# Performance work log

Hardware: AMD Instinct MI355X
Metric: run time of the kernel (lower is better)

The kernel has to match this reference:

```python
import jax, jax.numpy as jnp
import numpy as np

T = 32.0                       # softmax temperature
THRESH = float(np.cos(np.pi * 40.0 / 180.0))  # cos(degree), degree=40
NEG_INF = -9.0e15


def setup_inputs() -> dict:
    key = jax.random.key(0)
    ks = jax.random.split(key, 11)
    B, C, D_IMG, D_ATT, H_ATT, H = 2048, 1000, 2048, 312, 128, 128
    def rn(k, shape, scale=1.0):
        return jax.random.normal(k, shape, dtype=jnp.float32) * scale
    return {
        "image_feats": rn(ks[0], (B, D_IMG)),
        "img_proto":   rn(ks[1], (C, D_IMG)),
        "attributes":  rn(ks[2], (C, D_ATT)),
        "unused":      0,
        # parameters
        "att_g":   rn(ks[3], (D_ATT, H_ATT), 0.05),
        "slim_w":  rn(ks[4], (D_IMG, D_ATT), 0.02),   # proto_slim weight (transposed torch layout)
        "slim_b":  rn(ks[5], (D_ATT,), 0.02),
        "img_w":   rn(ks[6], (D_IMG, H), 0.02),
        "proto_w": rn(ks[7], (2 * D_ATT, H), 0.02),   # att_dim + proto_red_dim = 624
        "proto_b": rn(ks[8], (1, H), 0.02),
        "fc_w":    rn(ks[9], (H, 1), 0.05),
        "fc_b":    rn(ks[10], (1,), 0.05),
    }


def reference(image_feats, img_proto, attributes, unused,
              att_g, slim_w, slim_b, img_w, proto_w, proto_b, fc_w, fc_b):
    # proto_slim: [C, D_img] -> [C, att_dim]
    proto_red = img_proto @ slim_w + slim_b

    # --- get_attention: cosine similarity among attribute projections ---
    g = attributes @ att_g                                   # [C, att_hC] (g == h in original)
    gn = g / jnp.clip(jnp.linalg.norm(g, axis=1, keepdims=True), 1e-12)
    sim = gn @ gn.T                                          # [C, C] cosine similarity
    raw = jnp.where(sim > THRESH, sim, NEG_INF)              # threshold mask
    attn = jax.nn.softmax(raw * T, axis=1)                   # [C, C]

    # --- propagate prototypes ---
    att_outs = attn @ attributes                             # [C, att_dim]
    img_proto_outs = attn @ proto_red                        # [C, att_dim]
    outs = jnp.concatenate([att_outs, img_proto_outs], axis=1)  # [C, 2*att_dim]

    # --- relation MLP (broadcast instead of materialized expand+matmul) ---
    img_h = image_feats @ img_w                              # [B, H]
    proto_h = outs @ proto_w                                 # [C, H]
    hidden = jax.nn.relu(img_h[:, None, :] + proto_h[None, :, :] + proto_b)  # [B, C, H]
    outputs = hidden @ fc_w + fc_b                           # [B, C, 1]
    return outputs[..., 0]                                   # [B, C]
```

## Files before the change

kernel.cpp:

```cpp
#include <hip/hip_runtime.h>

typedef unsigned short ushort_t;
typedef __bf16 bf16x8 __attribute__((ext_vector_type(8)));
typedef float f32x4 __attribute__((ext_vector_type(4)));
typedef float f32x2 __attribute__((ext_vector_type(2)));
typedef ushort_t us4 __attribute__((ext_vector_type(4)));

#define T_SOFT 32.0f
#define THRESH 0.76604444311897803f
#define SW 1048
#define SO 648

__device__ __forceinline__ ushort_t f2bf(float f) {
  union { float f; unsigned u; } x; x.f = f;
  unsigned r = (x.u + 0x7fffu + ((x.u >> 16) & 1u)) >> 16;
  return (ushort_t)r;
}
__device__ __forceinline__ float bf2f(ushort_t h) {
  union { unsigned u; float f; } x; x.u = ((unsigned)h) << 16; return x.f;
}

__device__ __forceinline__ us4 pack4(float4 x) {
  union { unsigned u[2]; us4 h; } r;
  union { float4 f; unsigned u[4]; } a;
  a.f = x;
  r.u[0] = __builtin_amdgcn_perm(a.u[1] + 0x8000u, a.u[0] + 0x8000u, 0x07060302u);
  r.u[1] = __builtin_amdgcn_perm(a.u[3] + 0x8000u, a.u[2] + 0x8000u, 0x07060302u);
  return r.h;
}

__global__ __launch_bounds__(256) void tr3_k(const float* __restrict__ s0, ushort_t* __restrict__ d0,
                                             const float* __restrict__ s1, ushort_t* __restrict__ d1,
                                             const float* __restrict__ s2, ushort_t* __restrict__ d2,
                                             const float* __restrict__ s3, ushort_t* __restrict__ d3,
                                             ushort_t* __restrict__ gn_bf, ushort_t* __restrict__ poutT) {
  int b = blockIdx.x, tid = threadIdx.x;
  if (b >= 1296) {
    us4 z = {0, 0, 0, 0};
    if (b == 1296) {
      *reinterpret_cast<us4*>(gn_bf + 1000 * 128 + tid * 4) = z;
    } else {
      ushort_t* base = poutT + 632ull * 1024 + tid * 32;
      #pragma unroll
      for (int i = 0; i < 8; ++i) *reinterpret_cast<us4*>(base + i * 4) = z;
    }
    return;
  }
  __shared__ float tl[32][33];
  const float* src; ushort_t* dst; int R, C, Cw, Rpad, local, ctiles;
  if (b < 640)       { src = s0; dst = d0; R = 2048; C = 312; Cw = 320; Rpad = 2048; local = b;       ctiles = 10; }
  else if (b < 896)  { src = s1; dst = d1; R = 2048; C = 128; Cw = 128; Rpad = 2048; local = b - 640; ctiles = 4;  }
  else if (b < 976)  { src = s2; dst = d2; R = 624;  C = 128; Cw = 128; Rpad = 640;  local = b - 896; ctiles = 4;  }
  else               { src = s3; dst = d3; R = 1000; C = 312; Cw = 312; Rpad = 1024; local = b - 976; ctiles = 10; }
  int rt = local / ctiles, ct = local - rt * ctiles;
  int r0 = rt * 32, c0 = ct * 32;
  #pragma unroll
  for (int p = 0; p < 4; ++p) {
    int idx = p * 256 + tid;
    int rr = idx >> 5, cc = idx & 31;
    float v = 0.f;
    if (r0 + rr < R && c0 + cc < C) v = src[(size_t)(r0 + rr) * C + (c0 + cc)];
    tl[cc][rr] = v;
  }
  __syncthreads();
  int cc = tid >> 3, rq = tid & 7;
  if (c0 + cc < Cw) {
    us4 o;
    o[0] = f2bf(tl[cc][rq * 4 + 0]);
    o[1] = f2bf(tl[cc][rq * 4 + 1]);
    o[2] = f2bf(tl[cc][rq * 4 + 2]);
    o[3] = f2bf(tl[cc][rq * 4 + 3]);
    *reinterpret_cast<us4*>(dst + (size_t)(c0 + cc) * Rpad + r0 + rq * 4) = o;
  }
}

__device__ __forceinline__ void gemm_imgh(const float* __restrict__ A, const ushort_t* __restrict__ BT,
                                          float* __restrict__ C, int r0,
                                          ushort_t* __restrict__ As, ushort_t* __restrict__ Bs, int tid) {
  const int SA = 72;
  int lane = tid & 63, wv = tid >> 6;
  int l15 = lane & 15, quad = lane >> 4;
  int arow = tid >> 4, akq = tid & 15;
  int brow = tid >> 3, bkq = tid & 7;
  const float* agp[8];
  #pragma unroll
  for (int p = 0; p < 8; ++p) agp[p] = A + (size_t)(r0 + arow + p * 16) * 2048 + akq * 4;
  const ushort_t* bgp[4];
  #pragma unroll
  for (int p = 0; p < 4; ++p) bgp[p] = BT + (size_t)(brow + p * 32) * 2048 + bkq * 8;

  float4 ap[8]; bf16x8 bp[4];
  #pragma unroll
  for (int p = 0; p < 8; ++p) ap[p] = *reinterpret_cast<const float4*>(agp[p]);
  #pragma unroll
  for (int p = 0; p < 4; ++p) bp[p] = *reinterpret_cast<const bf16x8*>(bgp[p]);

  f32x4 acc[2][8];
  #pragma unroll
  for (int i = 0; i < 2; ++i)
    #pragma unroll
    for (int j = 0; j < 8; ++j) acc[i][j] = f32x4{0.f, 0.f, 0.f, 0.f};

  for (int s = 0; s < 32; ++s) {
    if (s) __syncthreads();
    #pragma unroll
    for (int p = 0; p < 8; ++p)
      *reinterpret_cast<us4*>(As + (arow + p * 16) * SA + akq * 4) = pack4(ap[p]);
    #pragma unroll
    for (int p = 0; p < 4; ++p)
      *reinterpret_cast<bf16x8*>(Bs + (brow + p * 32) * SA + bkq * 8) = bp[p];
    if (s + 1 < 32) {
      #pragma unroll
      for (int p = 0; p < 8; ++p) ap[p] = *reinterpret_cast<const float4*>(agp[p] + 64);
      #pragma unroll
      for (int p = 0; p < 4; ++p) bp[p] = *reinterpret_cast<const bf16x8*>(bgp[p] + 64);
      #pragma unroll
      for (int p = 0; p < 8; ++p) agp[p] += 64;
      #pragma unroll
      for (int p = 0; p < 4; ++p) bgp[p] += 64;
    }
    __syncthreads();
    #pragma unroll
    for (int kh = 0; kh < 2; ++kh) {
      bf16x8 af[2];
      #pragma unroll
      for (int pi = 0; pi < 2; ++pi)
        af[pi] = *reinterpret_cast<bf16x8*>(As + ((wv * 2 + pi) * 16 + l15) * SA + kh * 32 + quad * 8);
      #pragma unroll
      for (int ct = 0; ct < 8; ++ct) {
        bf16x8 bfr = *reinterpret_cast<bf16x8*>(Bs + (ct * 16 + l15) * SA + kh * 32 + quad * 8);
        acc[0][ct] = __builtin_amdgcn_mfma_f32_16x16x32_bf16(af[0], bfr, acc[0][ct], 0, 0, 0);
        acc[1][ct] = __builtin_amdgcn_mfma_f32_16x16x32_bf16(af[1], bfr, acc[1][ct], 0, 0, 0);
      }
    }
  }
  #pragma unroll
  for (int pi = 0; pi < 2; ++pi)
    #pragma unroll
    for (int ct = 0; ct < 8; ++ct) {
      int col = ct * 16 + l15;
      #pragma unroll
      for (int r = 0; r < 4; ++r) {
        int row = r0 + (wv * 2 + pi) * 16 + quad * 4 + r;
        C[(size_t)row * 128 + col] = acc[pi][ct][r];
      }
    }
}

__device__ __forceinline__ void gemm_protoT(const ushort_t* __restrict__ A, const float* __restrict__ B,
                                            ushort_t* __restrict__ poutT, int r0, int c0,
                                            ushort_t* __restrict__ As, ushort_t* __restrict__ Bs, int tid) {
  const int SA = 72;
  int lane = tid & 63, wv = tid >> 6;
  int l15 = lane & 15, quad = lane >> 4;
  int frow = tid >> 4, fkq = tid & 15;
  int hrow = tid >> 3, hkq = tid & 7;
  const ushort_t* agp[4];
  #pragma unroll
  for (int p = 0; p < 4; ++p) {
    int r = r0 + hrow + p * 32; if (r >= 320) r = 319;
    agp[p] = A + (size_t)r * 2048 + hkq * 8;
  }
  const float* bgp[8];
  #pragma unroll
  for (int p = 0; p < 8; ++p) {
    int n = c0 + frow + p * 16; if (n >= 1000) n = 999;
    bgp[p] = B + (size_t)n * 2048 + fkq * 4;
  }
  bf16x8 ar[4]; float4 br[8];
  #pragma unroll
  for (int p = 0; p < 4; ++p) ar[p] = *reinterpret_cast<const bf16x8*>(agp[p]);
  #pragma unroll
  for (int p = 0; p < 8; ++p) br[p] = *reinterpret_cast<const float4*>(bgp[p]);

  f32x4 acc[2][8];
  #pragma unroll
  for (int i = 0; i < 2; ++i)
    #pragma unroll
    for (int j = 0; j < 8; ++j) acc[i][j] = f32x4{0.f, 0.f, 0.f, 0.f};

  for (int s = 0; s < 32; ++s) {
    if (s) __syncthreads();
    #pragma unroll
    for (int p = 0; p < 4; ++p)
      *reinterpret_cast<bf16x8*>(As + (hrow + p * 32) * SA + hkq * 8) = ar[p];
    #pragma unroll
    for (int p = 0; p < 8; ++p)
      *reinterpret_cast<us4*>(Bs + (frow + p * 16) * SA + fkq * 4) = pack4(br[p]);
    if (s + 1 < 32) {
      #pragma unroll
      for (int p = 0; p < 4; ++p) ar[p] = *reinterpret_cast<const bf16x8*>(agp[p] + 64);
      #pragma unroll
      for (int p = 0; p < 8; ++p) br[p] = *reinterpret_cast<const float4*>(bgp[p] + 64);
      #pragma unroll
      for (int p = 0; p < 4; ++p) agp[p] += 64;
      #pragma unroll
      for (int p = 0; p < 8; ++p) bgp[p] += 64;
    }
    __syncthreads();
    #pragma unroll
    for (int kh = 0; kh < 2; ++kh) {
      bf16x8 af[2];
      #pragma unroll
      for (int pi = 0; pi < 2; ++pi)
        af[pi] = *reinterpret_cast<bf16x8*>(As + ((wv * 2 + pi) * 16 + l15) * SA + kh * 32 + quad * 8);
      #pragma unroll
      for (int ct = 0; ct < 8; ++ct) {
        bf16x8 bfr = *reinterpret_cast<bf16x8*>(Bs + (ct * 16 + l15) * SA + kh * 32 + quad * 8);
        acc[0][ct] = __builtin_amdgcn_mfma_f32_16x16x32_bf16(af[0], bfr, acc[0][ct], 0, 0, 0);
        acc[1][ct] = __builtin_amdgcn_mfma_f32_16x16x32_bf16(af[1], bfr, acc[1][ct], 0, 0, 0);
      }
    }
  }
  #pragma unroll
  for (int pi = 0; pi < 2; ++pi)
    #pragma unroll
    for (int ct = 0; ct < 8; ++ct) {
      int n = c0 + ct * 16 + l15;
      if (n < 1000) {
        #pragma unroll
        for (int r = 0; r < 4; ++r) {
          int m = r0 + (wv * 2 + pi) * 16 + quad * 4 + r;
          if (m < 320) poutT[(size_t)(312 + m) * 1024 + n] = f2bf(acc[pi][ct][r]);
        }
      }
    }
}

__global__ __launch_bounds__(256) void mega_k(
    const float* __restrict__ attributes, const float* __restrict__ att_g,
    ushort_t* __restrict__ gn_bf,
    const float* __restrict__ img_proto, const ushort_t* __restrict__ slimT,
    const float* __restrict__ image_feats, const ushort_t* __restrict__ imgwT,
    float* __restrict__ img_h, ushort_t* __restrict__ poutT) {
  __shared__ ushort_t As[128 * 72];
  __shared__ ushort_t Bs[128 * 72];
  int b = blockIdx.x, tid = threadIdx.x;
  if (b < 125) {
    __shared__ float a_lds[8][316];
    __shared__ float red2[8][2];
    int h = tid & 127;
    int c0 = b * 8;
    for (int idx = tid; idx < 8 * 312; idx += 256) {
      int r = idx / 312;
      int k = idx - r * 312;
      a_lds[r][k] = attributes[(c0 + r) * 312 + k];
    }
    __syncthreads();
    float acc[8] = {0.f,0.f,0.f,0.f,0.f,0.f,0.f,0.f};
    for (int k = 0; k < 312; k += 4) {
      float w0 = att_g[(k + 0) * 128 + h];
      float w1 = att_g[(k + 1) * 128 + h];
      float w2 = att_g[(k + 2) * 128 + h];
      float w3 = att_g[(k + 3) * 128 + h];
      #pragma unroll
      for (int r = 0; r < 8; ++r) {
        float4 a4 = *reinterpret_cast<const float4*>(&a_lds[r][k]);
        acc[r] += a4.x * w0 + a4.y * w1 + a4.z * w2 + a4.w * w3;
      }
    }
    int lane = tid & 63, wvid = (tid >> 6) & 1;
    #pragma unroll
    for (int r = 0; r < 8; ++r) {
      float v = acc[r] * acc[r];
      #pragma unroll
      for (int off = 32; off > 0; off >>= 1) v += __shfl_xor(v, off, 64);
      if (lane == 0) red2[r][wvid] = v;
    }
    __syncthreads();
    #pragma unroll
    for (int r = 0; r < 8; ++r) {
      float nrm = fmaxf(sqrtf(red2[r][0] + red2[r][1]), 1e-12f);
      gn_bf[(c0 + r) * 128 + h] = f2bf(acc[r] / nrm);
    }
    return;
  }
  b -= 125;
  if (b < 16) {
    gemm_imgh(image_feats, imgwT, img_h, b * 128, As, Bs, tid);
  } else {
    b -= 16;
    int rb = b >> 3, cb = b & 7;
    gemm_protoT(slimT, img_proto, poutT, rb * 128, cb * 128, As, Bs, tid);
  }
}

__global__ __launch_bounds__(256) void attn4_k(
    const ushort_t* __restrict__ gn_bf, const ushort_t* __restrict__ poutT,
    const float* __restrict__ slim_b, const ushort_t* __restrict__ protowT,
    const float* __restrict__ proto_b, float* __restrict__ ph) {
  __shared__ ushort_t W[16 * SW];
  __shared__ ushort_t OS[16 * SO];
  __shared__ float rsum[16];
  __shared__ int flags[63];
  int tid = threadIdx.x;
  int i0 = blockIdx.x * 16;
  int lane = tid & 63, wv = tid >> 6;
  int l15 = lane & 15, quad = lane >> 4;
  if (tid < 63) flags[tid] = 0;
  if (tid >= 64 && tid < 80) rsum[tid - 64] = 0.f;
  W[(tid >> 4) * SW + 1008 + (tid & 15)] = 0;
  __syncthreads();

  const ushort_t* abase = gn_bf + (size_t)(i0 + l15) * 128 + quad * 8;
  bf16x8 af0 = *reinterpret_cast<const bf16x8*>(abase);
  bf16x8 af1 = *reinterpret_cast<const bf16x8*>(abase + 32);
  bf16x8 af2 = *reinterpret_cast<const bf16x8*>(abase + 64);
  bf16x8 af3 = *reinterpret_cast<const bf16x8*>(abase + 96);
  float rs[4] = {0.f, 0.f, 0.f, 0.f};
  for (int jt = wv; jt < 63; jt += 4) {
    const ushort_t* bbase = gn_bf + (size_t)(jt * 16 + l15) * 128 + quad * 8;
    f32x4 d = {0.f, 0.f, 0.f, 0.f};
    d = __builtin_amdgcn_mfma_f32_16x16x32_bf16(af0, *reinterpret_cast<const bf16x8*>(bbase),      d, 0, 0, 0);
    d = __builtin_amdgcn_mfma_f32_16x16x32_bf16(af1, *reinterpret_cast<const bf16x8*>(bbase + 32), d, 0, 0, 0);
    d = __builtin_amdgcn_mfma_f32_16x16x32_bf16(af2, *reinterpret_cast<const bf16x8*>(bbase + 64), d, 0, 0, 0);
    d = __builtin_amdgcn_mfma_f32_16x16x32_bf16(af3, *reinterpret_cast<const bf16x8*>(bbase + 96), d, 0, 0, 0);
    int hot = 0;
    #pragma unroll
    for (int r = 0; r < 4; ++r) {
      float w = 0.f;
      if (d[r] > THRESH) { w = __expf(T_SOFT * (d[r] - 1.0f)); hot = 1; }
      ushort_t wb = f2bf(w);
      W[(quad * 4 + r) * SW + jt * 16 + l15] = wb;
      rs[r] += bf2f(wb);
    }
    if (hot) flags[jt] = 1;
  }
  #pragma unroll
  for (int r = 0; r < 4; ++r) {
    float v = rs[r];
    v += __shfl_xor(v, 1, 64); v += __shfl_xor(v, 2, 64);
    v += __shfl_xor(v, 4, 64); v += __shfl_xor(v, 8, 64);
    if (l15 == 0) atomicAdd(&rsum[quad * 4 + r], v);
  }
  __syncthreads();

  f32x4 acc[10];
  #pragma unroll
  for (int t = 0; t < 10; ++t) acc[t] = f32x4{0.f, 0.f, 0.f, 0.f};
  for (int s = 0; s < 32; ++s) {
    int f = flags[2 * s] | ((2 * s + 1 < 63) ? flags[2 * s + 1] : 0);
    if (!f) continue;
    bf16x8 a = *reinterpret_cast<bf16x8*>(W + l15 * SW + s * 32 + quad * 8);
    #pragma unroll
    for (int t = 0; t < 10; ++t) {
      int nrow = (wv * 10 + t) * 16 + l15;
      bf16x8 bfr = *reinterpret_cast<const bf16x8*>(poutT + (size_t)nrow * 1024 + s * 32 + quad * 8);
      acc[t] = __builtin_amdgcn_mfma_f32_16x16x32_bf16(a, bfr, acc[t], 0, 0, 0);
    }
  }
  #pragma unroll
  for (int t = 0; t < 10; ++t) {
    int col = (wv * 10 + t) * 16 + l15;
    float bias = (col >= 312 && col < 624) ? slim_b[col - 312] : 0.f;
    #pragma unroll
    for (int r = 0; r < 4; ++r) {
      int row = quad * 4 + r;
      float inv = 1.f / fmaxf(rsum[row], 1e-30f);
      OS[row * SO + col] = f2bf(acc[t][r] * inv + bias);
    }
  }
  __syncthreads();

  f32x4 acc2[2];
  acc2[0] = f32x4{0.f, 0.f, 0.f, 0.f};
  acc2[1] = f32x4{0.f, 0.f, 0.f, 0.f};
  for (int s = 0; s < 20; ++s) {
    bf16x8 a = *reinterpret_cast<bf16x8*>(OS + l15 * SO + s * 32 + quad * 8);
    #pragma unroll
    for (int t = 0; t < 2; ++t) {
      int n = (wv * 2 + t) * 16 + l15;
      bf16x8 bfr = *reinterpret_cast<const bf16x8*>(protowT + (size_t)n * 640 + s * 32 + quad * 8);
      acc2[t] = __builtin_amdgcn_mfma_f32_16x16x32_bf16(a, bfr, acc2[t], 0, 0, 0);
    }
  }
  #pragma unroll
  for (int t = 0; t < 2; ++t) {
    int h = (wv * 2 + t) * 16 + l15;
    float pb = proto_b[h];
    #pragma unroll
    for (int r = 0; r < 4; ++r) {
      int gi = i0 + quad * 4 + r;
      if (gi < 1000) ph[(size_t)gi * 128 + h] = acc2[t][r] + pb;
    }
  }
}

__global__ __launch_bounds__(256) void final_k(
    const float* __restrict__ img_h, const float* __restrict__ ph,
    const float* __restrict__ fc_w, const float* __restrict__ fc_b,
    float* __restrict__ out) {
  __shared__ float ih[128][132];
  __shared__ float ps[64][132];
  __shared__ float ws_[128];
  int tid = threadIdx.x;
  int b0 = blockIdx.x * 128;
  int c0 = blockIdx.y * 64;
  for (int idx = tid; idx < 4096; idx += 256) {
    int row = idx >> 5, c4 = (idx & 31) * 4;
    float4 v = *reinterpret_cast<const float4*>(img_h + (size_t)(b0 + row) * 128 + c4);
    *reinterpret_cast<float4*>(&ih[row][c4]) = v;
  }
  for (int idx = tid; idx < 2048; idx += 256) {
    int row = idx >> 5, c4 = (idx & 31) * 4;
    int c = c0 + row;
    float4 v = make_float4(0.f, 0.f, 0.f, 0.f);
    if (c < 1000) v = *reinterpret_cast<const float4*>(ph + (size_t)c * 128 + c4);
    *reinterpret_cast<float4*>(&ps[row][c4]) = v;
  }
  if (tid < 128) ws_[tid] = fc_w[tid];
  __syncthreads();
  int tx = tid & 15, ty = tid >> 4;
  f32x2 acc[8][4] = {};
  const f32x2 zero2 = {0.f, 0.f};
  for (int h = 0; h < 128; h += 4) {
    float4 w4 = *reinterpret_cast<float4*>(&ws_[h]);
    f32x2 wlo = {w4.x, w4.y}, whi = {w4.z, w4.w};
    float4 a4[8], p4[4];
    #pragma unroll
    for (int i = 0; i < 8; ++i) a4[i] = *reinterpret_cast<float4*>(&ih[ty * 8 + i][h]);
    #pragma unroll
    for (int j = 0; j < 4; ++j) p4[j] = *reinterpret_cast<float4*>(&ps[tx * 4 + j][h]);
    #pragma unroll
    for (int i = 0; i < 8; ++i) {
      f32x2 alo = {a4[i].x, a4[i].y}, ahi = {a4[i].z, a4[i].w};
      #pragma unroll
      for (int j = 0; j < 4; ++j) {
        f32x2 plo = {p4[j].x, p4[j].y}, phi = {p4[j].z, p4[j].w};
        f32x2 t0 = __builtin_elementwise_max(alo + plo, zero2);
        f32x2 t1 = __builtin_elementwise_max(ahi + phi, zero2);
        acc[i][j] = acc[i][j] + t0 * wlo;
        acc[i][j] = acc[i][j] + t1 * whi;
      }
    }
  }
  float fb = fc_b[0];
  #pragma unroll
  for (int i = 0; i < 8; ++i) {
    int b = b0 + ty * 8 + i;
    int c = c0 + tx * 4;
    if (c < 1000) {
      float4 v = make_float4(acc[i][0].x + acc[i][0].y + fb, acc[i][1].x + acc[i][1].y + fb,
                             acc[i][2].x + acc[i][2].y + fb, acc[i][3].x + acc[i][3].y + fb);
      *reinterpret_cast<float4*>(out + (size_t)b * 1000 + c) = v;
    }
  }
}

extern "C" void kernel_launch(void* const* d_in, const int* in_sizes, int n_in,
                              void* d_out, int out_size, void* d_ws, size_t ws_size,
                              hipStream_t stream) {
  const float* image_feats = (const float*)d_in[0];
  const float* img_proto   = (const float*)d_in[1];
  const float* attributes  = (const float*)d_in[2];
  const float* att_g   = (const float*)d_in[4];
  const float* slim_w  = (const float*)d_in[5];
  const float* slim_b  = (const float*)d_in[6];
  const float* img_w   = (const float*)d_in[7];
  const float* proto_w = (const float*)d_in[8];
  const float* proto_b = (const float*)d_in[9];
  const float* fc_w    = (const float*)d_in[10];
  const float* fc_b    = (const float*)d_in[11];
  float* out = (float*)d_out;

  char* ws = (char*)d_ws;
  size_t o = 0;
  auto alloc = [&](size_t bytes) { size_t r = o; o += (bytes + 255) & ~(size_t)255; return r; };
  ushort_t* imgwT   = (ushort_t*)(ws + alloc(128ull * 2048 * 2));
  ushort_t* slimT   = (ushort_t*)(ws + alloc(320ull * 2048 * 2));
  ushort_t* protowT = (ushort_t*)(ws + alloc(128ull * 640 * 2));
  ushort_t* gn_bf   = (ushort_t*)(ws + alloc(1008ull * 128 * 2));
  ushort_t* poutT   = (ushort_t*)(ws + alloc(640ull * 1024 * 2));
  float* img_h     = (float*)(ws + alloc(2048ull * 128 * 4));
  float* ph        = (float*)(ws + alloc(1000ull * 128 * 4));

  tr3_k<<<1298, 256, 0, stream>>>(slim_w, slimT, img_w, imgwT, proto_w, protowT,
                                  attributes, poutT, gn_bf, poutT);

  mega_k<<<165, 256, 0, stream>>>(attributes, att_g, gn_bf,
                                  img_proto, slimT,
                                  image_feats, imgwT, img_h, poutT);

  attn4_k<<<63, 256, 0, stream>>>(gn_bf, poutT, slim_b, protowT, proto_b, ph);

  final_k<<<dim3(16, 16), 256, 0, stream>>>(img_h, ph, fc_w, fc_b, out);
}
```

Baseline: 178.4 us.

## Split-K the image and prototype GEMMs with atomic accumulation

Splits the K=2048 reduction of the img_h and prototype-slim GEMMs into four chunks, so mega_k launches 285 blocks instead of 165 and fills more of the GPU's compute units. Partial results are combined with float atomicAdd into zeroed buffers, and a new conversion kernel packs the prototype accumulator into bf16 poutT. This costs two memsets, an extra kernel launch, atomic traffic, and a small amount of nondeterminism in the summation order.

```diff
diff --git a/kernel.cpp b/kernel.cpp
--- a/kernel.cpp
+++ b/kernel.cpp
@@ -75,7 +75,7 @@
 }
 
 __device__ __forceinline__ void gemm_imgh(const float* __restrict__ A, const ushort_t* __restrict__ BT,
-                                          float* __restrict__ C, int r0,
+                                          float* __restrict__ C, int r0, int k0,
                                           ushort_t* __restrict__ As, ushort_t* __restrict__ Bs, int tid) {
   const int SA = 72;
   int lane = tid & 63, wv = tid >> 6;
@@ -84,10 +84,10 @@
   int brow = tid >> 3, bkq = tid & 7;
   const float* agp[8];
   #pragma unroll
-  for (int p = 0; p < 8; ++p) agp[p] = A + (size_t)(r0 + arow + p * 16) * 2048 + akq * 4;
+  for (int p = 0; p < 8; ++p) agp[p] = A + (size_t)(r0 + arow + p * 16) * 2048 + k0 + akq * 4;
   const ushort_t* bgp[4];
   #pragma unroll
-  for (int p = 0; p < 4; ++p) bgp[p] = BT + (size_t)(brow + p * 32) * 2048 + bkq * 8;
+  for (int p = 0; p < 4; ++p) bgp[p] = BT + (size_t)(brow + p * 32) * 2048 + k0 + bkq * 8;
 
   float4 ap[8]; bf16x8 bp[4];
   #pragma unroll
@@ -101,7 +101,7 @@
     #pragma unroll
     for (int j = 0; j < 8; ++j) acc[i][j] = f32x4{0.f, 0.f, 0.f, 0.f};
 
-  for (int s = 0; s < 32; ++s) {
+  for (int s = 0; s < 8; ++s) {
     if (s) __syncthreads();
     #pragma unroll
     for (int p = 0; p < 8; ++p)
@@ -109,7 +109,7 @@
     #pragma unroll
     for (int p = 0; p < 4; ++p)
       *reinterpret_cast<bf16x8*>(Bs + (brow + p * 32) * SA + bkq * 8) = bp[p];
-    if (s + 1 < 32) {
+    if (s + 1 < 8) {
       #pragma unroll
       for (int p = 0; p < 8; ++p) ap[p] = *reinterpret_cast<const float4*>(agp[p] + 64);
       #pragma unroll
@@ -142,13 +142,13 @@
       #pragma unroll
       for (int r = 0; r < 4; ++r) {
         int row = r0 + (wv * 2 + pi) * 16 + quad * 4 + r;
-        C[(size_t)row * 128 + col] = acc[pi][ct][r];
+        atomicAdd(&C[(size_t)row * 128 + col], acc[pi][ct][r]);
       }
     }
 }
 
 __device__ __forceinline__ void gemm_protoT(const ushort_t* __restrict__ A, const float* __restrict__ B,
-                                            ushort_t* __restrict__ poutT, int r0, int c0,
+                                            float* __restrict__ pacc, int r0, int c0, int k0,
                                             ushort_t* __restrict__ As, ushort_t* __restrict__ Bs, int tid) {
   const int SA = 72;
   int lane = tid & 63, wv = tid >> 6;
@@ -159,13 +159,13 @@
   #pragma unroll
   for (int p = 0; p < 4; ++p) {
     int r = r0 + hrow + p * 32; if (r >= 320) r = 319;
-    agp[p] = A + (size_t)r * 2048 + hkq * 8;
+    agp[p] = A + (size_t)r * 2048 + k0 + hkq * 8;
   }
   const float* bgp[8];
   #pragma unroll
   for (int p = 0; p < 8; ++p) {
     int n = c0 + frow + p * 16; if (n >= 1000) n = 999;
-    bgp[p] = B + (size_t)n * 2048 + fkq * 4;
+    bgp[p] = B + (size_t)n * 2048 + k0 + fkq * 4;
   }
   bf16x8 ar[4]; float4 br[8];
   #pragma unroll
@@ -179,7 +179,7 @@
     #pragma unroll
     for (int j = 0; j < 8; ++j) acc[i][j] = f32x4{0.f, 0.f, 0.f, 0.f};
 
-  for (int s = 0; s < 32; ++s) {
+  for (int s = 0; s < 8; ++s) {
     if (s) __syncthreads();
     #pragma unroll
     for (int p = 0; p < 4; ++p)
@@ -187,7 +187,7 @@
     #pragma unroll
     for (int p = 0; p < 8; ++p)
       *reinterpret_cast<us4*>(Bs + (frow + p * 16) * SA + fkq * 4) = pack4(br[p]);
-    if (s + 1 < 32) {
+    if (s + 1 < 8) {
       #pragma unroll
       for (int p = 0; p < 4; ++p) ar[p] = *reinterpret_cast<const bf16x8*>(agp[p] + 64);
       #pragma unroll
@@ -221,7 +221,7 @@
         #pragma unroll
         for (int r = 0; r < 4; ++r) {
           int m = r0 + (wv * 2 + pi) * 16 + quad * 4 + r;
-          if (m < 320) poutT[(size_t)(312 + m) * 1024 + n] = f2bf(acc[pi][ct][r]);
+          if (m < 320) atomicAdd(&pacc[(size_t)m * 1024 + n], acc[pi][ct][r]);
         }
       }
     }
@@ -232,7 +232,7 @@
     ushort_t* __restrict__ gn_bf,
     const float* __restrict__ img_proto, const ushort_t* __restrict__ slimT,
     const float* __restrict__ image_feats, const ushort_t* __restrict__ imgwT,
-    float* __restrict__ img_h, ushort_t* __restrict__ poutT) {
+    float* __restrict__ img_h, float* __restrict__ pout_acc) {
   __shared__ ushort_t As[128 * 72];
   __shared__ ushort_t Bs[128 * 72];
   int b = blockIdx.x, tid = threadIdx.x;
@@ -276,13 +276,21 @@
     return;
   }
   b -= 125;
-  if (b < 16) {
-    gemm_imgh(image_feats, imgwT, img_h, b * 128, As, Bs, tid);
+  if (b < 64) {
+    int tile = b >> 2, kc = b & 3;
+    gemm_imgh(image_feats, imgwT, img_h, tile * 128, kc * 512, As, Bs, tid);
   } else {
-    b -= 16;
-    int rb = b >> 3, cb = b & 7;
-    gemm_protoT(slimT, img_proto, poutT, rb * 128, cb * 128, As, Bs, tid);
-  }
+    b -= 64;
+    int tile = b >> 2, kc = b & 3;
+    int rb = tile >> 3, cb = tile & 7;
+    gemm_protoT(slimT, img_proto, pout_acc, rb * 128, cb * 128, kc * 512, As, Bs, tid);
+  }
+}
+
+__global__ __launch_bounds__(256) void conv_k(const float* __restrict__ pacc, ushort_t* __restrict__ poutT) {
+  int idx = (blockIdx.x * 256 + threadIdx.x) * 4;
+  float4 v = *reinterpret_cast<const float4*>(pacc + idx);
+  *reinterpret_cast<us4*>(poutT + 312ull * 1024 + idx) = pack4(v);
 }
 
 __global__ __launch_bounds__(256) void attn4_k(
@@ -473,13 +481,19 @@
   ushort_t* poutT   = (ushort_t*)(ws + alloc(640ull * 1024 * 2));
   float* img_h     = (float*)(ws + alloc(2048ull * 128 * 4));
   float* ph        = (float*)(ws + alloc(1000ull * 128 * 4));
+  float* pout_acc  = (float*)(ws + alloc(320ull * 1024 * 4));
+
+  hipMemsetAsync(img_h, 0, 2048ull * 128 * 4, stream);
+  hipMemsetAsync(pout_acc, 0, 320ull * 1024 * 4, stream);
 
   tr3_k<<<1298, 256, 0, stream>>>(slim_w, slimT, img_w, imgwT, proto_w, protowT,
                                   attributes, poutT, gn_bf, poutT);
 
-  mega_k<<<165, 256, 0, stream>>>(attributes, att_g, gn_bf,
+  mega_k<<<285, 256, 0, stream>>>(attributes, att_g, gn_bf,
                                   img_proto, slimT,
-                                  image_feats, imgwT, img_h, poutT);
+                                  image_feats, imgwT, img_h, pout_acc);
+
+  conv_k<<<320, 256, 0, stream>>>(pout_acc, poutT);
 
   attn4_k<<<63, 256, 0, stream>>>(gn_bf, poutT, slim_b, protowT, proto_b, ph);
 
```

New measurement: 178.3 us. No clear change (-0.1%).

## Reassociate proto projection before attention and split-K GEMMs with atomics

Applied to the files above, without the earlier changes.

The proto_w projection is now applied before the attention matmul, computing G = outs_pre @ proto_w in a new kernel. This shrinks the attention propagation from a 640-wide output to a 128-wide output, and the slim bias is folded into a precomputed bias vector. The img_h and proto_red GEMMs are split along K into 8 chunks accumulated with float atomics into zeroed buffers, which raises parallelism from 16+ blocks to hundreds. The final kernel moves to 512 threads with fewer rows per thread. The change adds two more launches, atomic traffic and a zeroing pass, and alters the bf16 rounding order.

```diff
diff --git a/kernel.cpp b/kernel.cpp
--- a/kernel.cpp
+++ b/kernel.cpp
@@ -9,7 +9,6 @@
 #define T_SOFT 32.0f
 #define THRESH 0.76604444311897803f
 #define SW 1048
-#define SO 648
 
 __device__ __forceinline__ ushort_t f2bf(float f) {
   union { float f; unsigned u; } x; x.f = f;
@@ -32,17 +31,24 @@
 __global__ __launch_bounds__(256) void tr3_k(const float* __restrict__ s0, ushort_t* __restrict__ d0,
                                              const float* __restrict__ s1, ushort_t* __restrict__ d1,
                                              const float* __restrict__ s2, ushort_t* __restrict__ d2,
-                                             const float* __restrict__ s3, ushort_t* __restrict__ d3,
-                                             ushort_t* __restrict__ gn_bf, ushort_t* __restrict__ poutT) {
+                                             const float* __restrict__ attributes, ushort_t* __restrict__ poutN,
+                                             ushort_t* __restrict__ gn_bf, float* __restrict__ zero_base) {
   int b = blockIdx.x, tid = threadIdx.x;
-  if (b >= 1296) {
-    us4 z = {0, 0, 0, 0};
-    if (b == 1296) {
+  if (b >= 976) {
+    if (b < 1288) {
+      int t = (b - 976) * 256 + tid;
+      int row = t / 78, c4 = (t - row * 78) * 4;
+      us4 v = {0, 0, 0, 0};
+      if (row < 1000) v = pack4(*reinterpret_cast<const float4*>(attributes + (size_t)row * 312 + c4));
+      *reinterpret_cast<us4*>(poutN + (size_t)row * 640 + c4) = v;
+    } else if (b < 1432) {
+      int t = (b - 1288) * 256 + tid;
+      float4* zp = reinterpret_cast<float4*>(zero_base) + (size_t)t * 4;
+      float4 z = make_float4(0.f, 0.f, 0.f, 0.f);
+      zp[0] = z; zp[1] = z; zp[2] = z; zp[3] = z;
+    } else {
+      us4 z = {0, 0, 0, 0};
       *reinterpret_cast<us4*>(gn_bf + 1000 * 128 + tid * 4) = z;
-    } else {
-      ushort_t* base = poutT + 632ull * 1024 + tid * 32;
-      #pragma unroll
-      for (int i = 0; i < 8; ++i) *reinterpret_cast<us4*>(base + i * 4) = z;
     }
     return;
   }
@@ -50,8 +56,7 @@
   const float* src; ushort_t* dst; int R, C, Cw, Rpad, local, ctiles;
   if (b < 640)       { src = s0; dst = d0; R = 2048; C = 312; Cw = 320; Rpad = 2048; local = b;       ctiles = 10; }
   else if (b < 896)  { src = s1; dst = d1; R = 2048; C = 128; Cw = 128; Rpad = 2048; local = b - 640; ctiles = 4;  }
-  else if (b < 976)  { src = s2; dst = d2; R = 624;  C = 128; Cw = 128; Rpad = 640;  local = b - 896; ctiles = 4;  }
-  else               { src = s3; dst = d3; R = 1000; C = 312; Cw = 312; Rpad = 1024; local = b - 976; ctiles = 10; }
+  else               { src = s2; dst = d2; R = 624;  C = 128; Cw = 128; Rpad = 640;  local = b - 896; ctiles = 4;  }
   int rt = local / ctiles, ct = local - rt * ctiles;
   int r0 = rt * 32, c0 = ct * 32;
   #pragma unroll
@@ -75,7 +80,7 @@
 }
 
 __device__ __forceinline__ void gemm_imgh(const float* __restrict__ A, const ushort_t* __restrict__ BT,
-                                          float* __restrict__ C, int r0,
+                                          float* __restrict__ C, int r0, int k0,
                                           ushort_t* __restrict__ As, ushort_t* __restrict__ Bs, int tid) {
   const int SA = 72;
   int lane = tid & 63, wv = tid >> 6;
@@ -84,10 +89,10 @@
   int brow = tid >> 3, bkq = tid & 7;
   const float* agp[8];
   #pragma unroll
-  for (int p = 0; p < 8; ++p) agp[p] = A + (size_t)(r0 + arow + p * 16) * 2048 + akq * 4;
+  for (int p = 0; p < 8; ++p) agp[p] = A + (size_t)(r0 + arow + p * 16) * 2048 + k0 + akq * 4;
   const ushort_t* bgp[4];
   #pragma unroll
-  for (int p = 0; p < 4; ++p) bgp[p] = BT + (size_t)(brow + p * 32) * 2048 + bkq * 8;
+  for (int p = 0; p < 4; ++p) bgp[p] = BT + (size_t)(brow + p * 32) * 2048 + k0 + bkq * 8;
 
   float4 ap[8]; bf16x8 bp[4];
   #pragma unroll
@@ -101,7 +106,7 @@
     #pragma unroll
     for (int j = 0; j < 8; ++j) acc[i][j] = f32x4{0.f, 0.f, 0.f, 0.f};
 
-  for (int s = 0; s < 32; ++s) {
+  for (int s = 0; s < 4; ++s) {
     if (s) __syncthreads();
     #pragma unroll
     for (int p = 0; p < 8; ++p)
@@ -109,7 +114,7 @@
     #pragma unroll
     for (int p = 0; p < 4; ++p)
       *reinterpret_cast<bf16x8*>(Bs + (brow + p * 32) * SA + bkq * 8) = bp[p];
-    if (s + 1 < 32) {
+    if (s + 1 < 4) {
       #pragma unroll
       for (int p = 0; p < 8; ++p) ap[p] = *reinterpret_cast<const float4*>(agp[p] + 64);
       #pragma unroll
@@ -142,36 +147,36 @@
       #pragma unroll
       for (int r = 0; r < 4; ++r) {
         int row = r0 + (wv * 2 + pi) * 16 + quad * 4 + r;
-        C[(size_t)row * 128 + col] = acc[pi][ct][r];
-      }
-    }
-}
-
-__device__ __forceinline__ void gemm_protoT(const ushort_t* __restrict__ A, const float* __restrict__ B,
-                                            ushort_t* __restrict__ poutT, int r0, int c0,
-                                            ushort_t* __restrict__ As, ushort_t* __restrict__ Bs, int tid) {
+        atomicAdd(&C[(size_t)row * 128 + col], acc[pi][ct][r]);
+      }
+    }
+}
+
+__device__ __forceinline__ void gemm_proto(const float* __restrict__ A, const ushort_t* __restrict__ BT,
+                                           float* __restrict__ pacc2, int r0, int c0, int k0,
+                                           ushort_t* __restrict__ As, ushort_t* __restrict__ Bs, int tid) {
   const int SA = 72;
   int lane = tid & 63, wv = tid >> 6;
   int l15 = lane & 15, quad = lane >> 4;
-  int frow = tid >> 4, fkq = tid & 15;
-  int hrow = tid >> 3, hkq = tid & 7;
-  const ushort_t* agp[4];
+  int arow = tid >> 4, akq = tid & 15;
+  int brow = tid >> 3, bkq = tid & 7;
+  const float* agp[8];
+  #pragma unroll
+  for (int p = 0; p < 8; ++p) {
+    int r = r0 + arow + p * 16; if (r >= 1000) r = 999;
+    agp[p] = A + (size_t)r * 2048 + k0 + akq * 4;
+  }
+  const ushort_t* bgp[4];
   #pragma unroll
   for (int p = 0; p < 4; ++p) {
-    int r = r0 + hrow + p * 32; if (r >= 320) r = 319;
-    agp[p] = A + (size_t)r * 2048 + hkq * 8;
-  }
-  const float* bgp[8];
-  #pragma unroll
-  for (int p = 0; p < 8; ++p) {
-    int n = c0 + frow + p * 16; if (n >= 1000) n = 999;
-    bgp[p] = B + (size_t)n * 2048 + fkq * 4;
-  }
-  bf16x8 ar[4]; float4 br[8];
-  #pragma unroll
-  for (int p = 0; p < 4; ++p) ar[p] = *reinterpret_cast<const bf16x8*>(agp[p]);
-  #pragma unroll
-  for (int p = 0; p < 8; ++p) br[p] = *reinterpret_cast<const float4*>(bgp[p]);
+    int n = c0 + brow + p * 32; if (n >= 320) n = 319;
+    bgp[p] = BT + (size_t)n * 2048 + k0 + bkq * 8;
+  }
+  float4 ap[8]; bf16x8 bp[4];
+  #pragma unroll
+  for (int p = 0; p < 8; ++p) ap[p] = *reinterpret_cast<const float4*>(agp[p]);
+  #pragma unroll
+  for (int p = 0; p < 4; ++p) bp[p] = *reinterpret_cast<const bf16x8*>(bgp[p]);
 
   f32x4 acc[2][8];
   #pragma unroll
@@ -179,23 +184,23 @@
     #pragma unroll
     for (int j = 0; j < 8; ++j) acc[i][j] = f32x4{0.f, 0.f, 0.f, 0.f};
 
-  for (int s = 0; s < 32; ++s) {
+  for (int s = 0; s < 4; ++s) {
     if (s) __syncthreads();
     #pragma unroll
+    for (int p = 0; p < 8; ++p)
+      *reinterpret_cast<us4*>(As + (arow + p * 16) * SA + akq * 4) = pack4(ap[p]);
+    #pragma unroll
     for (int p = 0; p < 4; ++p)
-      *reinterpret_cast<bf16x8*>(As + (hrow + p * 32) * SA + hkq * 8) = ar[p];
-    #pragma unroll
-    for (int p = 0; p < 8; ++p)
-      *reinterpret_cast<us4*>(Bs + (frow + p * 16) * SA + fkq * 4) = pack4(br[p]);
-    if (s + 1 < 32) {
-      #pragma unroll
-      for (int p = 0; p < 4; ++p) ar[p] = *reinterpret_cast<const bf16x8*>(agp[p] + 64);
-      #pragma unroll
-      for (int p = 0; p < 8; ++p) br[p] = *reinterpret_cast<const float4*>(bgp[p] + 64);
-      #pragma unroll
-      for (int p = 0; p < 4; ++p) agp[p] += 64;
-      #pragma unroll
-      for (int p = 0; p < 8; ++p) bgp[p] += 64;
+      *reinterpret_cast<bf16x8*>(Bs + (brow + p * 32) * SA + bkq * 8) = bp[p];
+    if (s + 1 < 4) {
+      #pragma unroll
+      for (int p = 0; p < 8; ++p) ap[p] = *reinterpret_cast<const float4*>(agp[p] + 64);
+      #pragma unroll
+      for (int p = 0; p < 4; ++p) bp[p] = *reinterpret_cast<const bf16x8*>(bgp[p] + 64);
+      #pragma unroll
+      for (int p = 0; p < 8; ++p) agp[p] += 64;
+      #pragma unroll
+      for (int p = 0; p < 4; ++p) bgp[p] += 64;
     }
     __syncthreads();
     #pragma unroll
@@ -216,12 +221,12 @@
   for (int pi = 0; pi < 2; ++pi)
     #pragma unroll
     for (int ct = 0; ct < 8; ++ct) {
-      int n = c0 + ct * 16 + l15;
-      if (n < 1000) {
+      int col = c0 + ct * 16 + l15;
+      if (col < 320) {
         #pragma unroll
         for (int r = 0; r < 4; ++r) {
-          int m = r0 + (wv * 2 + pi) * 16 + quad * 4 + r;
-          if (m < 320) poutT[(size_t)(312 + m) * 1024 + n] = f2bf(acc[pi][ct][r]);
+          int row = r0 + (wv * 2 + pi) * 16 + quad * 4 + r;
+          atomicAdd(&pacc2[(size_t)row * 320 + col], acc[pi][ct][r]);
         }
       }
     }
@@ -232,7 +237,7 @@
     ushort_t* __restrict__ gn_bf,
     const float* __restrict__ img_proto, const ushort_t* __restrict__ slimT,
     const float* __restrict__ image_feats, const ushort_t* __restrict__ imgwT,
-    float* __restrict__ img_h, ushort_t* __restrict__ poutT) {
+    float* __restrict__ img_h, float* __restrict__ pacc2) {
   __shared__ ushort_t As[128 * 72];
   __shared__ ushort_t Bs[128 * 72];
   int b = blockIdx.x, tid = threadIdx.x;
@@ -276,21 +281,113 @@
     return;
   }
   b -= 125;
-  if (b < 16) {
-    gemm_imgh(image_feats, imgwT, img_h, b * 128, As, Bs, tid);
+  if (b < 128) {
+    int tile = b >> 3, kc = b & 7;
+    gemm_imgh(image_feats, imgwT, img_h, tile * 128, kc * 256, As, Bs, tid);
   } else {
-    b -= 16;
-    int rb = b >> 3, cb = b & 7;
-    gemm_protoT(slimT, img_proto, poutT, rb * 128, cb * 128, As, Bs, tid);
-  }
-}
-
-__global__ __launch_bounds__(256) void attn4_k(
-    const ushort_t* __restrict__ gn_bf, const ushort_t* __restrict__ poutT,
-    const float* __restrict__ slim_b, const ushort_t* __restrict__ protowT,
-    const float* __restrict__ proto_b, float* __restrict__ ph) {
+    b -= 128;
+    int tile = b >> 3, kc = b & 7;
+    int rb = tile / 3, cb = tile - rb * 3;
+    gemm_proto(img_proto, slimT, pacc2, rb * 128, cb * 128, kc * 256, As, Bs, tid);
+  }
+}
+
+__global__ __launch_bounds__(256) void conv_k(const float* __restrict__ pacc2, ushort_t* __restrict__ poutN) {
+  int t = blockIdx.x * 256 + threadIdx.x;
+  int row = t / 82, m = (t - row * 82) * 4;
+  us4 v = {0, 0, 0, 0};
+  if (m < 320) v = pack4(*reinterpret_cast<const float4*>(pacc2 + (size_t)row * 320 + m));
+  *reinterpret_cast<us4*>(poutN + (size_t)row * 640 + 312 + m) = v;
+}
+
+__global__ __launch_bounds__(256) void g_k(const ushort_t* __restrict__ protowT, const ushort_t* __restrict__ poutN,
+                                           const float* __restrict__ proto_w, const float* __restrict__ slim_b,
+                                           const float* __restrict__ proto_b,
+                                           ushort_t* __restrict__ GT, float* __restrict__ biasG) {
+  int b = blockIdx.x, tid = threadIdx.x;
+  if (b >= 8) {
+    int h = tid & 127;
+    float acc = proto_b[h];
+    for (int n = 0; n < 312; n += 4) {
+      acc += slim_b[n + 0] * proto_w[(size_t)(312 + n) * 128 + h];
+      acc += slim_b[n + 1] * proto_w[(size_t)(313 + n) * 128 + h];
+      acc += slim_b[n + 2] * proto_w[(size_t)(314 + n) * 128 + h];
+      acc += slim_b[n + 3] * proto_w[(size_t)(315 + n) * 128 + h];
+    }
+    if (tid < 128) biasG[h] = acc;
+    return;
+  }
+  const int SA = 72;
+  __shared__ ushort_t As[128 * 72];
+  __shared__ ushort_t Bs[128 * 72];
+  int lane = tid & 63, wv = tid >> 6;
+  int l15 = lane & 15, quad = lane >> 4;
+  int hrow = tid >> 3, hkq = tid & 7;
+  size_t j0 = (size_t)b * 128;
+  const ushort_t* agp[4];
+  const ushort_t* bgp[4];
+  #pragma unroll
+  for (int p = 0; p < 4; ++p) {
+    agp[p] = protowT + (size_t)(hrow + p * 32) * 640 + hkq * 8;
+    bgp[p] = poutN + (j0 + hrow + p * 32) * 640 + hkq * 8;
+  }
+  bf16x8 ar[4], br[4];
+  #pragma unroll
+  for (int p = 0; p < 4; ++p) { ar[p] = *reinterpret_cast<const bf16x8*>(agp[p]); br[p] = *reinterpret_cast<const bf16x8*>(bgp[p]); }
+
+  f32x4 acc[2][8];
+  #pragma unroll
+  for (int i = 0; i < 2; ++i)
+    #pragma unroll
+    for (int j = 0; j < 8; ++j) acc[i][j] = f32x4{0.f, 0.f, 0.f, 0.f};
+
+  for (int s = 0; s < 10; ++s) {
+    if (s) __syncthreads();
+    #pragma unroll
+    for (int p = 0; p < 4; ++p) {
+      *reinterpret_cast<bf16x8*>(As + (hrow + p * 32) * SA + hkq * 8) = ar[p];
+      *reinterpret_cast<bf16x8*>(Bs + (hrow + p * 32) * SA + hkq * 8) = br[p];
+    }
+    if (s + 1 < 10) {
+      #pragma unroll
+      for (int p = 0; p < 4; ++p) {
+        ar[p] = *reinterpret_cast<const bf16x8*>(agp[p] + 64);
+        br[p] = *reinterpret_cast<const bf16x8*>(bgp[p] + 64);
+        agp[p] += 64; bgp[p] += 64;
+      }
+    }
+    __syncthreads();
+    #pragma unroll
+    for (int kh = 0; kh < 2; ++kh) {
+      bf16x8 af[2];
+      #pragma unroll
+      for (int pi = 0; pi < 2; ++pi)
+        af[pi] = *reinterpret_cast<bf16x8*>(As + ((wv * 2 + pi) * 16 + l15) * SA + kh * 32 + quad * 8);
+      #pragma unroll
+      for (int ct = 0; ct < 8; ++ct) {
+        bf16x8 bfr = *reinterpret_cast<bf16x8*>(Bs + (ct * 16 + l15) * SA + kh * 32 + quad * 8);
+        acc[0][ct] = __builtin_amdgcn_mfma_f32_16x16x32_bf16(af[0], bfr, acc[0][ct], 0, 0, 0);
+        acc[1][ct] = __builtin_amdgcn_mfma_f32_16x16x32_bf16(af[1], bfr, acc[1][ct], 0, 0, 0);
+      }
+    }
+  }
+  #pragma unroll
+  for (int pi = 0; pi < 2; ++pi)
+    #pragma unroll
+    for (int ct = 0; ct < 8; ++ct) {
+      int col = ct * 16 + l15;
+      #pragma unroll
+      for (int r = 0; r < 4; ++r) {
+        int row = (wv * 2 + pi) * 16 + quad * 4 + r;
+        GT[(size_t)row * 1024 + j0 + col] = f2bf(acc[pi][ct][r]);
+      }
+    }
+}
+
+__global__ __launch_bounds__(256) void attn5_k(
+    const ushort_t* __restrict__ gn_bf, const ushort_t* __restrict__ GT,
+    const float* __restrict__ biasG, float* __restrict__ ph) {
   __shared__ ushort_t W[16 * SW];
-  __shared__ ushort_t OS[16 * SO];
   __shared__ float rsum[16];
   __shared__ int flags[63];
   int tid = threadIdx.x;
@@ -335,58 +432,35 @@
   }
   __syncthreads();
 
-  f32x4 acc[10];
-  #pragma unroll
-  for (int t = 0; t < 10; ++t) acc[t] = f32x4{0.f, 0.f, 0.f, 0.f};
+  f32x4 acc2[2];
+  acc2[0] = f32x4{0.f, 0.f, 0.f, 0.f};
+  acc2[1] = f32x4{0.f, 0.f, 0.f, 0.f};
   for (int s = 0; s < 32; ++s) {
     int f = flags[2 * s] | ((2 * s + 1 < 63) ? flags[2 * s + 1] : 0);
     if (!f) continue;
     bf16x8 a = *reinterpret_cast<bf16x8*>(W + l15 * SW + s * 32 + quad * 8);
     #pragma unroll
-    for (int t = 0; t < 10; ++t) {
-      int nrow = (wv * 10 + t) * 16 + l15;
-      bf16x8 bfr = *reinterpret_cast<const bf16x8*>(poutT + (size_t)nrow * 1024 + s * 32 + quad * 8);
-      acc[t] = __builtin_amdgcn_mfma_f32_16x16x32_bf16(a, bfr, acc[t], 0, 0, 0);
-    }
-  }
-  #pragma unroll
-  for (int t = 0; t < 10; ++t) {
-    int col = (wv * 10 + t) * 16 + l15;
-    float bias = (col >= 312 && col < 624) ? slim_b[col - 312] : 0.f;
+    for (int t = 0; t < 2; ++t) {
+      int h = (wv * 2 + t) * 16 + l15;
+      bf16x8 bfr = *reinterpret_cast<const bf16x8*>(GT + (size_t)h * 1024 + s * 32 + quad * 8);
+      acc2[t] = __builtin_amdgcn_mfma_f32_16x16x32_bf16(a, bfr, acc2[t], 0, 0, 0);
+    }
+  }
+  #pragma unroll
+  for (int t = 0; t < 2; ++t) {
+    int h = (wv * 2 + t) * 16 + l15;
+    float bg = biasG[h];
     #pragma unroll
     for (int r = 0; r < 4; ++r) {
       int row = quad * 4 + r;
+      int gi = i0 + row;
       float inv = 1.f / fmaxf(rsum[row], 1e-30f);
-      OS[row * SO + col] = f2bf(acc[t][r] * inv + bias);
-    }
-  }
-  __syncthreads();
-
-  f32x4 acc2[2];
-  acc2[0] = f32x4{0.f, 0.f, 0.f, 0.f};
-  acc2[1] = f32x4{0.f, 0.f, 0.f, 0.f};
-  for (int s = 0; s < 20; ++s) {
-    bf16x8 a = *reinterpret_cast<bf16x8*>(OS + l15 * SO + s * 32 + quad * 8);
-    #pragma unroll
-    for (int t = 0; t < 2; ++t) {
-      int n = (wv * 2 + t) * 16 + l15;
-      bf16x8 bfr = *reinterpret_cast<const bf16x8*>(protowT + (size_t)n * 640 + s * 32 + quad * 8);
-      acc2[t] = __builtin_amdgcn_mfma_f32_16x16x32_bf16(a, bfr, acc2[t], 0, 0, 0);
-    }
-  }
-  #pragma unroll
-  for (int t = 0; t < 2; ++t) {
-    int h = (wv * 2 + t) * 16 + l15;
-    float pb = proto_b[h];
-    #pragma unroll
-    for (int r = 0; r < 4; ++r) {
-      int gi = i0 + quad * 4 + r;
-      if (gi < 1000) ph[(size_t)gi * 128 + h] = acc2[t][r] + pb;
-    }
-  }
-}
-
-__global__ __launch_bounds__(256) void final_k(
+      if (gi < 1000) ph[(size_t)gi * 128 + h] = acc2[t][r] * inv + bg;
+    }
+  }
+}
+
+__global__ __launch_bounds__(512) void final_k(
     const float* __restrict__ img_h, const float* __restrict__ ph,
     const float* __restrict__ fc_w, const float* __restrict__ fc_b,
     float* __restrict__ out) {
@@ -396,12 +470,12 @@
   int tid = threadIdx.x;
   int b0 = blockIdx.x * 128;
   int c0 = blockIdx.y * 64;
-  for (int idx = tid; idx < 4096; idx += 256) {
+  for (int idx = tid; idx < 4096; idx += 512) {
     int row = idx >> 5, c4 = (idx & 31) * 4;
     float4 v = *reinterpret_cast<const float4*>(img_h + (size_t)(b0 + row) * 128 + c4);
     *reinterpret_cast<float4*>(&ih[row][c4]) = v;
   }
-  for (int idx = tid; idx < 2048; idx += 256) {
+  for (int idx = tid; idx < 2048; idx += 512) {
     int row = idx >> 5, c4 = (idx & 31) * 4;
     int c = c0 + row;
     float4 v = make_float4(0.f, 0.f, 0.f, 0.f);
@@ -411,18 +485,18 @@
   if (tid < 128) ws_[tid] = fc_w[tid];
   __syncthreads();
   int tx = tid & 15, ty = tid >> 4;
-  f32x2 acc[8][4] = {};
+  f32x2 acc[4][4] = {};
   const f32x2 zero2 = {0.f, 0.f};
   for (int h = 0; h < 128; h += 4) {
     float4 w4 = *reinterpret_cast<float4*>(&ws_[h]);
     f32x2 wlo = {w4.x, w4.y}, whi = {w4.z, w4.w};
-    float4 a4[8], p4[4];
-    #pragma unroll
-    for (int i = 0; i < 8; ++i) a4[i] = *reinterpret_cast<float4*>(&ih[ty * 8 + i][h]);
+    float4 a4[4], p4[4];
+    #pragma unroll
+    for (int i = 0; i < 4; ++i) a4[i] = *reinterpret_cast<float4*>(&ih[ty * 4 + i][h]);
     #pragma unroll
     for (int j = 0; j < 4; ++j) p4[j] = *reinterpret_cast<float4*>(&ps[tx * 4 + j][h]);
     #pragma unroll
-    for (int i = 0; i < 8; ++i) {
+    for (int i = 0; i < 4; ++i) {
       f32x2 alo = {a4[i].x, a4[i].y}, ahi = {a4[i].z, a4[i].w};
       #pragma unroll
       for (int j = 0; j < 4; ++j) {
@@ -436,8 +510,8 @@
   }
   float fb = fc_b[0];
   #pragma unroll
-  for (int i = 0; i < 8; ++i) {
-    int b = b0 + ty * 8 + i;
+  for (int i = 0; i < 4; ++i) {
+    int b = b0 + ty * 4 + i;
     int c = c0 + tx * 4;
     if (c < 1000) {
       float4 v = make_float4(acc[i][0].x + acc[i][0].y + fb, acc[i][1].x + acc[i][1].y + fb,
@@ -470,18 +544,25 @@
   ushort_t* slimT   = (ushort_t*)(ws + alloc(320ull * 2048 * 2));
   ushort_t* protowT = (ushort_t*)(ws + alloc(128ull * 640 * 2));
   ushort_t* gn_bf   = (ushort_t*)(ws + alloc(1008ull * 128 * 2));
-  ushort_t* poutT   = (ushort_t*)(ws + alloc(640ull * 1024 * 2));
+  ushort_t* poutN   = (ushort_t*)(ws + alloc(1024ull * 640 * 2));
+  ushort_t* GT      = (ushort_t*)(ws + alloc(128ull * 1024 * 2));
+  float* biasG     = (float*)(ws + alloc(128ull * 4));
   float* img_h     = (float*)(ws + alloc(2048ull * 128 * 4));
+  float* pacc2     = (float*)(ws + alloc(1024ull * 320 * 4));
   float* ph        = (float*)(ws + alloc(1000ull * 128 * 4));
 
-  tr3_k<<<1298, 256, 0, stream>>>(slim_w, slimT, img_w, imgwT, proto_w, protowT,
-                                  attributes, poutT, gn_bf, poutT);
-
-  mega_k<<<165, 256, 0, stream>>>(attributes, att_g, gn_bf,
+  tr3_k<<<1433, 256, 0, stream>>>(slim_w, slimT, img_w, imgwT, proto_w, protowT,
+                                  attributes, poutN, gn_bf, img_h);
+
+  mega_k<<<445, 256, 0, stream>>>(attributes, att_g, gn_bf,
                                   img_proto, slimT,
-                                  image_feats, imgwT, img_h, poutT);
-
-  attn4_k<<<63, 256, 0, stream>>>(gn_bf, poutT, slim_b, protowT, proto_b, ph);
-
-  final_k<<<dim3(16, 16), 256, 0, stream>>>(img_h, ph, fc_w, fc_b, out);
-}
+                                  image_feats, imgwT, img_h, pacc2);
+
+  conv_k<<<328, 256, 0, stream>>>(pacc2, poutN);
+
+  g_k<<<9, 256, 0, stream>>>(protowT, poutN, proto_w, slim_b, proto_b, GT, biasG);
+
+  attn5_k<<<63, 256, 0, stream>>>(gn_bf, GT, biasG, ph);
+
+  final_k<<<dim3(16, 16), 512, 0, stream>>>(img_h, ph, fc_w, fc_b, out);
+}
```

Result: no change. 179.3 us (+0.5%).
